# Optimization experiments

Measured on AMD Instinct MI355X. Metric: run time of the kernel, lower is better.

Reference implementation:

```python
import jax, jax.numpy as jnp
import numpy as np

N_NODES = 100000
N_EDGES = 1600000


def setup_inputs() -> dict:
    key = jax.random.key(0)
    ks = jax.random.split(key, 10)
    return {
        "src": jax.random.randint(ks[0], (N_EDGES,), 0, N_NODES, dtype=jnp.int32),
        "dst": jax.random.randint(ks[1], (N_EDGES,), 0, N_NODES, dtype=jnp.int32),
        "logits": jax.random.normal(ks[2], (N_NODES, 64), jnp.float32),
        "features": jax.random.normal(ks[3], (N_NODES, 512), jnp.float32),
        "proj_W": jax.random.normal(ks[4], (512, 128), jnp.float32) * 0.04,
        "proj_b": jnp.zeros((128,), jnp.float32),
        "deg_table": jax.random.normal(ks[5], (512, 64), jnp.float32) * 0.1,
        "W1": jax.random.normal(ks[6], (256, 128), jnp.float32) * 0.06,
        "b1": jnp.zeros((128,), jnp.float32),
        "W2": jax.random.normal(ks[7], (128, 64), jnp.float32) * 0.09,
        "b2": jnp.zeros((64,), jnp.float32),
    }


def _graph_conv(x, W, b, src, dst, out_deg, in_deg, n):
    # DGL GraphConv, norm='both': scale src by out_deg^-1/2, SpMM sum over
    # edges (src -> dst), scale dst by in_deg^-1/2, then bias. Weight is
    # applied before aggregation when in_feats > out_feats (true here).
    cs = jax.lax.rsqrt(jnp.maximum(out_deg, 1.0))  # [N]
    cd = jax.lax.rsqrt(jnp.maximum(in_deg, 1.0))   # [N]
    h = x * cs[:, None]
    if W.shape[0] > W.shape[1]:
        h = h @ W
        agg = jax.ops.segment_sum(h[src], dst, num_segments=n)
    else:
        agg = jax.ops.segment_sum(h[src], dst, num_segments=n) @ W
    return agg * cd[:, None] + b


def reference(src, dst, logits, features, proj_W, proj_b, deg_table, W1, b1, W2, b2):
    n = logits.shape[0]
    ones = jnp.ones(src.shape, jnp.float32)
    out_deg = jax.ops.segment_sum(ones, src, num_segments=n)  # [N]
    in_deg = jax.ops.segment_sum(ones, dst, num_segments=n)   # [N]

    feat = features @ proj_W + proj_b                          # [N, 128]
    deg_idx = (in_deg + out_deg).astype(jnp.int32)             # [N]
    deg_emb = deg_table[deg_idx]                               # [N, 64]
    x = jnp.concatenate([logits, feat, deg_emb], axis=-1)      # [N, 256]

    x = _graph_conv(x, W1, b1, src, dst, out_deg, in_deg, n)
    x = jax.nn.relu(x)  # dropout omitted (eval mode)
    x = _graph_conv(x, W2, b2, src, dst, out_deg, in_deg, n)
    return x
```

## Files before the change

kernel.cpp:

```cpp
#include <hip/hip_runtime.h>
#include <cstdint>
#include <cstddef>


typedef short short8 __attribute__((ext_vector_type(8)));
typedef float f32x4 __attribute__((ext_vector_type(4)));

__device__ __forceinline__ unsigned short f2bf(float f) {
    unsigned u = __float_as_uint(f);
    u += 0x7fff + ((u >> 16) & 1);
    return (unsigned short)(u >> 16);
}
__device__ __forceinline__ float bf2f(unsigned short s) {
    return __uint_as_float(((unsigned)s) << 16);
}

__device__ __forceinline__ void split_f4(float4 a, float4 b, short8& hv, short8& lv) {
    float f[8] = {a.x, a.y, a.z, a.w, b.x, b.y, b.z, b.w};
#pragma unroll
    for (int i = 0; i < 8; ++i) {
        unsigned u = __float_as_uint(f[i]);
        hv[i] = (short)(u >> 16);
        float r = f[i] - __uint_as_float(u & 0xffff0000u);
        lv[i] = (short)(__float_as_uint(r) >> 16);
    }
}


__global__ __launch_bounds__(256) void k_bcount(
    const int* __restrict__ src, const int* __restrict__ dst, int E,
    int* __restrict__ dcount, int* __restrict__ scount)
{
    __shared__ int dh[128], sh_[128];
    int t = threadIdx.x;
    if (t < 128) { dh[t] = 0; sh_[t] = 0; }
    __syncthreads();
    int e0 = blockIdx.x * 4096;
#pragma unroll
    for (int i = 0; i < 16; ++i) {
        int idx = e0 + t + i * 256;
        if (idx < E) {
            atomicAdd(&dh[dst[idx] >> 10], 1);
            atomicAdd(&sh_[src[idx] >> 10], 1);
        }
    }
    __syncthreads();
    if (t < 128) {
        if (dh[t]) atomicAdd(&dcount[t], dh[t]);
        if (sh_[t]) atomicAdd(&scount[t], sh_[t]);
    }
}

__global__ __launch_bounds__(128) void k_bscan(
    const int* __restrict__ dcount, const int* __restrict__ scount, int nb,
    int E, int* __restrict__ dboff, int* __restrict__ sboff,
    int* __restrict__ dcur, int* __restrict__ scur,
    int* __restrict__ rowp, int N)
{
    __shared__ int sh[128];
    int t = threadIdx.x;
    int v = (t < nb) ? dcount[t] : 0;
    sh[t] = v;
    __syncthreads();
    for (int off = 1; off < 128; off <<= 1) {
        int x = (t >= off) ? sh[t - off] : 0;
        __syncthreads();
        sh[t] += x;
        __syncthreads();
    }
    if (t < nb) { int e = sh[t] - v; dboff[t] = e; dcur[t] = e; }
    __syncthreads();
    int v2 = (t < nb) ? scount[t] : 0;
    sh[t] = v2;
    __syncthreads();
    for (int off = 1; off < 128; off <<= 1) {
        int x = (t >= off) ? sh[t - off] : 0;
        __syncthreads();
        sh[t] += x;
        __syncthreads();
    }
    if (t < nb) { int e = sh[t] - v2; sboff[t] = e; scur[t] = e; }
    if (t == 0) rowp[N] = E;
}

__global__ __launch_bounds__(256) void k_scatter2(
    const int* __restrict__ src, const int* __restrict__ dst, int E,
    int* __restrict__ dcur, int* __restrict__ scur,
    unsigned* __restrict__ ebuf, unsigned short* __restrict__ sbuf, int nb)
{
    __shared__ int dh[128], dbase[128], sh_[128], sbase[128];
    int t = threadIdx.x;
    int e0 = blockIdx.x * 4096;
    if (t < 128) { dh[t] = 0; sh_[t] = 0; }
    __syncthreads();
    int s_[16], d_[16];
#pragma unroll
    for (int i = 0; i < 16; ++i) {
        int idx = e0 + t + i * 256;
        if (idx < E) {
            s_[i] = src[idx];
            d_[i] = dst[idx];
            atomicAdd(&dh[d_[i] >> 10], 1);
            atomicAdd(&sh_[s_[i] >> 10], 1);
        } else d_[i] = -1;
    }
    __syncthreads();
    if (t < nb) {
        if (dh[t]) dbase[t] = atomicAdd(&dcur[t], dh[t]);
        if (sh_[t]) sbase[t] = atomicAdd(&scur[t], sh_[t]);
    }
    __syncthreads();
    if (t < 128) { dh[t] = 0; sh_[t] = 0; }
    __syncthreads();
#pragma unroll
    for (int i = 0; i < 16; ++i) {
        if (d_[i] >= 0) {
            int b = d_[i] >> 10;
            int p = dbase[b] + atomicAdd(&dh[b], 1);
            ebuf[p] = (unsigned)s_[i] | ((unsigned)(d_[i] & 1023) << 17);
            int bs = s_[i] >> 10;
            int q = sbase[bs] + atomicAdd(&sh_[bs], 1);
            sbuf[q] = (unsigned short)(s_[i] & 1023);
        }
    }
}

__global__ __launch_bounds__(512) void k_bucket_dst(
    const unsigned* __restrict__ ebuf, const int* __restrict__ dboff,
    const int* __restrict__ dcount, int* __restrict__ ind,
    int* __restrict__ rowp, int* __restrict__ csr, int N)
{
    __shared__ int cnt[1024];
    __shared__ int sums[512];
    int b = blockIdx.x;
    int nb0 = b << 10;
    int ncnt = min(1024, N - nb0);
    int t = threadIdx.x;
    cnt[t] = 0; cnt[t + 512] = 0;
    __syncthreads();
    int lo = dboff[b], hi = lo + dcount[b];
    for (int idx = lo + t; idx < hi; idx += 512)
        atomicAdd(&cnt[ebuf[idx] >> 17], 1);
    __syncthreads();
    int c0 = cnt[2 * t], c1 = cnt[2 * t + 1];
    sums[t] = c0 + c1;
    __syncthreads();
    for (int off = 1; off < 512; off <<= 1) {
        int x = (t >= off) ? sums[t - off] : 0;
        __syncthreads();
        sums[t] += x;
        __syncthreads();
    }
    int excl = sums[t] - (c0 + c1);
    int r0 = lo + excl, r1 = r0 + c0;
    if (2 * t < ncnt)     { rowp[nb0 + 2 * t] = r0;     ind[nb0 + 2 * t] = c0; }
    if (2 * t + 1 < ncnt) { rowp[nb0 + 2 * t + 1] = r1; ind[nb0 + 2 * t + 1] = c1; }
    __syncthreads();
    cnt[2 * t] = r0; cnt[2 * t + 1] = r1;
    __syncthreads();
    for (int idx = lo + t; idx < hi; idx += 512) {
        unsigned e = ebuf[idx];
        int p = atomicAdd(&cnt[e >> 17], 1);
        csr[p] = (int)(e & 0x1FFFF);
    }
}

__global__ __launch_bounds__(512) void k_bucket_src(
    const unsigned short* __restrict__ sbuf, const int* __restrict__ sboff,
    const int* __restrict__ scount, int* __restrict__ outd, int N)
{
    __shared__ int cnt[1024];
    int b = blockIdx.x;
    int nb0 = b << 10;
    int ncnt = min(1024, N - nb0);
    int t = threadIdx.x;
    cnt[t] = 0; cnt[t + 512] = 0;
    __syncthreads();
    int lo = sboff[b], hi = lo + scount[b];
    for (int idx = lo + t; idx < hi; idx += 512)
        atomicAdd(&cnt[sbuf[idx]], 1);
    __syncthreads();
    if (t < ncnt) outd[nb0 + t] = cnt[t];
    if (t + 512 < ncnt) outd[nb0 + t + 512] = cnt[t + 512];
}

__global__ __launch_bounds__(256) void k_norms(
    const int* __restrict__ outd, const int* __restrict__ ind, int N,
    float* __restrict__ cs, float* __restrict__ cd, int* __restrict__ didx)
{
    int i = blockIdx.x * 256 + threadIdx.x;
    if (i < N) {
        int od = outd[i], id = ind[i];
        cs[i] = rsqrtf((float)(od > 0 ? od : 1));
        cd[i] = rsqrtf((float)(id > 0 ? id : 1));
        int d = od + id;
        didx[i] = d > 511 ? 511 : d;
    }
}

__global__ __launch_bounds__(256) void k_wf(
    const float* __restrict__ projW, const float* __restrict__ W1,
    float* __restrict__ WF)
{
    int idx = blockIdx.x * 256 + threadIdx.x;
    int k = idx >> 7, j = idx & 127;
    const float* a = projW + (size_t)k * 128;
    float s = 0.f;
#pragma unroll 8
    for (int m = 0; m < 128; ++m) s = fmaf(a[m], W1[(size_t)(64 + m) * 128 + j], s);
    WF[idx] = s;
}

__global__ void k_cb(const float* __restrict__ projb, const float* __restrict__ W1,
                     float* __restrict__ cb)
{
    int j = threadIdx.x;
    float s = 0.f;
    for (int m = 0; m < 128; ++m) s = fmaf(projb[m], W1[(size_t)(64 + m) * 128 + j], s);
    cb[j] = s;
}

__global__ __launch_bounds__(256) void k_wt1(
    const float* __restrict__ WF, const float* __restrict__ W1,
    unsigned short* __restrict__ wt_hi, unsigned short* __restrict__ wt_lo)
{
    int idx = blockIdx.x * 256 + threadIdx.x;
    int j = idx / 640, k = idx - j * 640;
    float v;
    if (k < 512) v = WF[(size_t)k * 128 + j];
    else if (k < 576) v = W1[(size_t)(k - 512) * 128 + j];
    else v = W1[(size_t)(192 + k - 576) * 128 + j];
    unsigned short h = f2bf(v);
    wt_hi[idx] = h;
    float r = v - bf2f(h);
    wt_lo[idx] = (unsigned short)(__float_as_uint(r) >> 16);
}

__global__ __launch_bounds__(256) void k_wt2(
    const float* __restrict__ W2,
    unsigned short* __restrict__ w2t_hi, unsigned short* __restrict__ w2t_lo)
{
    int idx = blockIdx.x * 256 + threadIdx.x;
    int j = idx >> 7, k = idx & 127;
    float v = W2[(size_t)k * 64 + j];
    unsigned short h = f2bf(v);
    w2t_hi[idx] = h;
    float r = v - bf2f(h);
    w2t_lo[idx] = (unsigned short)(__float_as_uint(r) >> 16);
}

__global__ __launch_bounds__(256, 2) void k_h1(
    const float* __restrict__ logits, const float* __restrict__ features,
    const float* __restrict__ deg_table, const int* __restrict__ didx,
    const unsigned short* __restrict__ wt_hi, const unsigned short* __restrict__ wt_lo,
    const float* __restrict__ cb, const float* __restrict__ cs,
    unsigned short* __restrict__ h1, int N)
{
    constexpr int NT = 20;
    __shared__ __align__(16) short Ah[2][128 * 32];
    __shared__ __align__(16) short Al[2][128 * 32];
    __shared__ __align__(16) short Bh[2][128 * 32];
    __shared__ __align__(16) short Bl[2][128 * 32];
    int tid = threadIdx.x;
    int i0 = blockIdx.x * 128;
    int sr = tid >> 1, shh = tid & 1;
    int snode = i0 + sr; if (snode >= N) snode = N - 1;
    int sdidx = didx[snode];
    int wo0 = sr * 32 + ((shh    ) ^ (sr & 3)) * 8;
    int wo1 = sr * 32 + ((shh + 2) ^ (sr & 3)) * 8;
    int lane = tid & 63, w = tid >> 6;
    int wr = w >> 1, wc = w & 1;
    int fr = lane & 15, kg = lane >> 4;
    int aoff = (wr * 64 + fr) * 32 + (kg ^ (fr & 3)) * 8;
    int boff = (wc * 64 + fr) * 32 + (kg ^ (fr & 3)) * 8;

    f32x4 acc[4][4];
#pragma unroll
    for (int ri = 0; ri < 4; ++ri)
#pragma unroll
        for (int ci = 0; ci < 4; ++ci) acc[ri][ci] = (f32x4)0.f;

    float4 fa0, fa1, fa2, fa3;
    uint4 pbh0, pbh1, pbl0, pbl1;

    auto loadT = [&](int t) {
        const float* ap;
        if (t < 16)      ap = features  + (size_t)snode * 512 + t * 32;
        else if (t < 18) ap = logits    + (size_t)snode * 64 + (t - 16) * 32;
        else             ap = deg_table + (size_t)sdidx * 64 + (t - 18) * 32;
        ap += shh * 8;
        fa0 = *(const float4*)(ap);
        fa1 = *(const float4*)(ap + 4);
        fa2 = *(const float4*)(ap + 16);
        fa3 = *(const float4*)(ap + 20);
        const unsigned short* bh = wt_hi + (size_t)sr * 640 + t * 32 + shh * 8;
        const unsigned short* bl = wt_lo + (size_t)sr * 640 + t * 32 + shh * 8;
        pbh0 = *(const uint4*)(bh);
        pbh1 = *(const uint4*)(bh + 16);
        pbl0 = *(const uint4*)(bl);
        pbl1 = *(const uint4*)(bl + 16);
    };
    auto writeT = [&](int buf) {
        short8 h0, l0, h1v, l1v;
        split_f4(fa0, fa1, h0, l0);
        split_f4(fa2, fa3, h1v, l1v);
        *(short8*)&Ah[buf][wo0] = h0;   *(short8*)&Ah[buf][wo1] = h1v;
        *(short8*)&Al[buf][wo0] = l0;   *(short8*)&Al[buf][wo1] = l1v;
        *(uint4*)&Bh[buf][wo0] = pbh0;  *(uint4*)&Bh[buf][wo1] = pbh1;
        *(uint4*)&Bl[buf][wo0] = pbl0;  *(uint4*)&Bl[buf][wo1] = pbl1;
    };

    loadT(0);
    writeT(0);
    __syncthreads();
    for (int t = 0; t < NT; ++t) {
        if (t + 1 < NT) loadT(t + 1);
        int cbuf = t & 1;
        short8 ah[4], al[4];
#pragma unroll
        for (int ri = 0; ri < 4; ++ri) {
            ah[ri] = *(const short8*)&Ah[cbuf][aoff + ri * 512];
            al[ri] = *(const short8*)&Al[cbuf][aoff + ri * 512];
        }
#pragma unroll
        for (int ci = 0; ci < 4; ++ci) {
            short8 bh = *(const short8*)&Bh[cbuf][boff + ci * 512];
            short8 bl = *(const short8*)&Bl[cbuf][boff + ci * 512];
#pragma unroll
            for (int ri = 0; ri < 4; ++ri) {
                acc[ri][ci] = __builtin_amdgcn_mfma_f32_16x16x32_bf16(ah[ri], bh, acc[ri][ci], 0, 0, 0);
                acc[ri][ci] = __builtin_amdgcn_mfma_f32_16x16x32_bf16(al[ri], bh, acc[ri][ci], 0, 0, 0);
                acc[ri][ci] = __builtin_amdgcn_mfma_f32_16x16x32_bf16(ah[ri], bl, acc[ri][ci], 0, 0, 0);
            }
        }
        if (t + 1 < NT) writeT((t + 1) & 1);
        __syncthreads();
    }

    float cbv[4];
#pragma unroll
    for (int ci = 0; ci < 4; ++ci) cbv[ci] = cb[wc * 64 + ci * 16 + fr];
#pragma unroll
    for (int ri = 0; ri < 4; ++ri) {
#pragma unroll
        for (int j = 0; j < 4; ++j) {
            int row = i0 + wr * 64 + ri * 16 + kg * 4 + j;
            if (row < N) {
                float scv = cs[row];
#pragma unroll
                for (int ci = 0; ci < 4; ++ci) {
                    int col = wc * 64 + ci * 16 + fr;
                    h1[(size_t)row * 128 + col] = f2bf(scv * (acc[ri][ci][j] + cbv[ci]));
                }
            }
        }
    }
}

__global__ __launch_bounds__(256) void k_agg1(
    const unsigned short* __restrict__ h1, const int* __restrict__ rowp,
    const int* __restrict__ csr, const float* __restrict__ cd,
    const float* __restrict__ b1, float* __restrict__ y, int N)
{
    int i = blockIdx.x * 4 + (threadIdx.x >> 6);
    if (i >= N) return;
    int lane = threadIdx.x & 63;
    int s0 = rowp[i], s1 = rowp[i + 1];
    float ax = 0.f, ay = 0.f;
    int e = s0;
    for (; e + 8 <= s1; e += 8) {
        unsigned u0 = *(const unsigned*)(h1 + (size_t)csr[e + 0] * 128 + lane * 2);
        unsigned u1 = *(const unsigned*)(h1 + (size_t)csr[e + 1] * 128 + lane * 2);
        unsigned u2 = *(const unsigned*)(h1 + (size_t)csr[e + 2] * 128 + lane * 2);
        unsigned u3 = *(const unsigned*)(h1 + (size_t)csr[e + 3] * 128 + lane * 2);
        unsigned u4 = *(const unsigned*)(h1 + (size_t)csr[e + 4] * 128 + lane * 2);
        unsigned u5 = *(const unsigned*)(h1 + (size_t)csr[e + 5] * 128 + lane * 2);
        unsigned u6 = *(const unsigned*)(h1 + (size_t)csr[e + 6] * 128 + lane * 2);
        unsigned u7 = *(const unsigned*)(h1 + (size_t)csr[e + 7] * 128 + lane * 2);
        ax += ((__uint_as_float(u0 << 16) + __uint_as_float(u1 << 16)) +
               (__uint_as_float(u2 << 16) + __uint_as_float(u3 << 16))) +
              ((__uint_as_float(u4 << 16) + __uint_as_float(u5 << 16)) +
               (__uint_as_float(u6 << 16) + __uint_as_float(u7 << 16)));
        ay += ((__uint_as_float(u0 & 0xffff0000u) + __uint_as_float(u1 & 0xffff0000u)) +
               (__uint_as_float(u2 & 0xffff0000u) + __uint_as_float(u3 & 0xffff0000u))) +
              ((__uint_as_float(u4 & 0xffff0000u) + __uint_as_float(u5 & 0xffff0000u)) +
               (__uint_as_float(u6 & 0xffff0000u) + __uint_as_float(u7 & 0xffff0000u)));
    }
    for (; e < s1; ++e) {
        unsigned u = *(const unsigned*)(h1 + (size_t)csr[e] * 128 + lane * 2);
        ax += __uint_as_float(u << 16);
        ay += __uint_as_float(u & 0xffff0000u);
    }
    float cdi = cd[i];
    float2 o;
    o.x = fmaxf(fmaf(ax, cdi, b1[lane * 2 + 0]), 0.f);
    o.y = fmaxf(fmaf(ay, cdi, b1[lane * 2 + 1]), 0.f);
    *(float2*)(y + (size_t)i * 128 + lane * 2) = o;
}

__global__ __launch_bounds__(256, 2) void k_h2(
    const float* __restrict__ y,
    const unsigned short* __restrict__ w2t_hi, const unsigned short* __restrict__ w2t_lo,
    const float* __restrict__ cs, unsigned short* __restrict__ h2, int N)
{
    constexpr int NT = 4;
    __shared__ __align__(16) short Ah[2][128 * 32];
    __shared__ __align__(16) short Al[2][128 * 32];
    __shared__ __align__(16) short Bh[2][64 * 32];
    __shared__ __align__(16) short Bl[2][64 * 32];
    int tid = threadIdx.x;
    int i0 = blockIdx.x * 128;
    int sr = tid >> 1, shh = tid & 1;
    int snode = i0 + sr; if (snode >= N) snode = N - 1;
    const float* abase = y + (size_t)snode * 128 + shh * 8;
    int awo0 = sr * 32 + ((shh    ) ^ (sr & 3)) * 8;
    int awo1 = sr * 32 + ((shh + 2) ^ (sr & 3)) * 8;
    int brow_s = tid >> 2, bc = tid & 3;
    int bwo = brow_s * 32 + (bc ^ (brow_s & 3)) * 8;
    int lane = tid & 63, w = tid >> 6;
    int wr = w >> 1, wc = w & 1;
    int fr = lane & 15, kg = lane >> 4;
    int aoff = (wr * 64 + fr) * 32 + (kg ^ (fr & 3)) * 8;
    int boff = (wc * 32 + fr) * 32 + (kg ^ (fr & 3)) * 8;

    f32x4 acc[4][2];
#pragma unroll
    for (int ri = 0; ri < 4; ++ri)
#pragma unroll
        for (int ci = 0; ci < 2; ++ci) acc[ri][ci] = (f32x4)0.f;

    float4 fa0, fa1, fa2, fa3;
    uint4 pbh0, pbl0;

    auto loadT = [&](int t) {
        const float* ap = abase + t * 32;
        fa0 = *(const float4*)(ap);
        fa1 = *(const float4*)(ap + 4);
        fa2 = *(const float4*)(ap + 16);
        fa3 = *(const float4*)(ap + 20);
        pbh0 = *(const uint4*)(w2t_hi + (size_t)brow_s * 128 + t * 32 + bc * 8);
        pbl0 = *(const uint4*)(w2t_lo + (size_t)brow_s * 128 + t * 32 + bc * 8);
    };
    auto writeT = [&](int buf) {
        short8 h0, l0, h1v, l1v;
        split_f4(fa0, fa1, h0, l0);
        split_f4(fa2, fa3, h1v, l1v);
        *(short8*)&Ah[buf][awo0] = h0;  *(short8*)&Ah[buf][awo1] = h1v;
        *(short8*)&Al[buf][awo0] = l0;  *(short8*)&Al[buf][awo1] = l1v;
        *(uint4*)&Bh[buf][bwo] = pbh0;
        *(uint4*)&Bl[buf][bwo] = pbl0;
    };

    loadT(0);
    writeT(0);
    __syncthreads();
    for (int t = 0; t < NT; ++t) {
        if (t + 1 < NT) loadT(t + 1);
        int cbuf = t & 1;
        short8 ah[4], al[4];
#pragma unroll
        for (int ri = 0; ri < 4; ++ri) {
            ah[ri] = *(const short8*)&Ah[cbuf][aoff + ri * 512];
            al[ri] = *(const short8*)&Al[cbuf][aoff + ri * 512];
        }
#pragma unroll
        for (int ci = 0; ci < 2; ++ci) {
            short8 bh = *(const short8*)&Bh[cbuf][boff + ci * 512];
            short8 bl = *(const short8*)&Bl[cbuf][boff + ci * 512];
#pragma unroll
            for (int ri = 0; ri < 4; ++ri) {
                acc[ri][ci] = __builtin_amdgcn_mfma_f32_16x16x32_bf16(ah[ri], bh, acc[ri][ci], 0, 0, 0);
                acc[ri][ci] = __builtin_amdgcn_mfma_f32_16x16x32_bf16(al[ri], bh, acc[ri][ci], 0, 0, 0);
                acc[ri][ci] = __builtin_amdgcn_mfma_f32_16x16x32_bf16(ah[ri], bl, acc[ri][ci], 0, 0, 0);
            }
        }
        if (t + 1 < NT) writeT((t + 1) & 1);
        __syncthreads();
    }

#pragma unroll
    for (int ri = 0; ri < 4; ++ri) {
#pragma unroll
        for (int j = 0; j < 4; ++j) {
            int row = i0 + wr * 64 + ri * 16 + kg * 4 + j;
            if (row < N) {
                float scv = cs[row];
#pragma unroll
                for (int ci = 0; ci < 2; ++ci) {
                    int col = wc * 32 + ci * 16 + fr;
                    h2[(size_t)row * 64 + col] = f2bf(scv * acc[ri][ci][j]);
                }
            }
        }
    }
}

__global__ __launch_bounds__(256) void k_agg2(
    const unsigned short* __restrict__ h2, const int* __restrict__ rowp,
    const int* __restrict__ csr, const float* __restrict__ cd,
    const float* __restrict__ b2, float* __restrict__ out, int N)
{
    int i = blockIdx.x * 8 + (threadIdx.x >> 5);
    if (i >= N) return;
    int lane = threadIdx.x & 31;
    int s0 = rowp[i], s1 = rowp[i + 1];
    float ax = 0.f, ay = 0.f;
    int e = s0;
    for (; e + 8 <= s1; e += 8) {
        unsigned u0 = *(const unsigned*)(h2 + (size_t)csr[e + 0] * 64 + lane * 2);
        unsigned u1 = *(const unsigned*)(h2 + (size_t)csr[e + 1] * 64 + lane * 2);
        unsigned u2 = *(const unsigned*)(h2 + (size_t)csr[e + 2] * 64 + lane * 2);
        unsigned u3 = *(const unsigned*)(h2 + (size_t)csr[e + 3] * 64 + lane * 2);
        unsigned u4 = *(const unsigned*)(h2 + (size_t)csr[e + 4] * 64 + lane * 2);
        unsigned u5 = *(const unsigned*)(h2 + (size_t)csr[e + 5] * 64 + lane * 2);
        unsigned u6 = *(const unsigned*)(h2 + (size_t)csr[e + 6] * 64 + lane * 2);
        unsigned u7 = *(const unsigned*)(h2 + (size_t)csr[e + 7] * 64 + lane * 2);
        ax += ((__uint_as_float(u0 << 16) + __uint_as_float(u1 << 16)) +
               (__uint_as_float(u2 << 16) + __uint_as_float(u3 << 16))) +
              ((__uint_as_float(u4 << 16) + __uint_as_float(u5 << 16)) +
               (__uint_as_float(u6 << 16) + __uint_as_float(u7 << 16)));
        ay += ((__uint_as_float(u0 & 0xffff0000u) + __uint_as_float(u1 & 0xffff0000u)) +
               (__uint_as_float(u2 & 0xffff0000u) + __uint_as_float(u3 & 0xffff0000u))) +
              ((__uint_as_float(u4 & 0xffff0000u) + __uint_as_float(u5 & 0xffff0000u)) +
               (__uint_as_float(u6 & 0xffff0000u) + __uint_as_float(u7 & 0xffff0000u)));
    }
    for (; e < s1; ++e) {
        unsigned u = *(const unsigned*)(h2 + (size_t)csr[e] * 64 + lane * 2);
        ax += __uint_as_float(u << 16);
        ay += __uint_as_float(u & 0xffff0000u);
    }
    float cdi = cd[i];
    float2 o;
    o.x = fmaf(ax, cdi, b2[lane * 2 + 0]);
    o.y = fmaf(ay, cdi, b2[lane * 2 + 1]);
    *(float2*)(out + (size_t)i * 64 + lane * 2) = o;
}

extern "C" void kernel_launch(void* const* d_in, const int* in_sizes, int n_in,
                              void* d_out, int out_size, void* d_ws, size_t ws_size,
                              hipStream_t stream)
{
    const int* src = (const int*)d_in[0];
    const int* dst = (const int*)d_in[1];
    const float* logits = (const float*)d_in[2];
    const float* features = (const float*)d_in[3];
    const float* projW = (const float*)d_in[4];
    const float* projb = (const float*)d_in[5];
    const float* deg_table = (const float*)d_in[6];
    const float* W1 = (const float*)d_in[7];
    const float* b1 = (const float*)d_in[8];
    const float* W2 = (const float*)d_in[9];
    const float* b2 = (const float*)d_in[10];
    const int E = in_sizes[0];
    const int N = in_sizes[2] / 64;

    char* base = (char*)d_ws;
    size_t off = 0;
    auto alloc = [&](size_t bytes) -> void* {
        void* p = base + off;
        off += (bytes + 255) & ~(size_t)255;
        return p;
    };
    int* outd   = (int*)alloc((size_t)N * 4);
    int* ind    = (int*)alloc((size_t)N * 4);
    int* rowp   = (int*)alloc((size_t)(N + 1) * 4);
    int* csr    = (int*)alloc((size_t)E * 4);
    unsigned* ebuf = (unsigned*)alloc((size_t)E * 4);
    unsigned short* sbuf = (unsigned short*)alloc((size_t)E * 2);
    int* didx   = (int*)alloc((size_t)N * 4);
    float* cs   = (float*)alloc((size_t)N * 4);
    float* cd   = (float*)alloc((size_t)N * 4);
    float* WF   = (float*)alloc((size_t)512 * 128 * 4);
    float* cb   = (float*)alloc((size_t)128 * 4);
    int* dcount = (int*)alloc(128 * 4);
    int* scount = (int*)alloc(128 * 4);
    int* dboff  = (int*)alloc(128 * 4);
    int* sboff  = (int*)alloc(128 * 4);
    int* dcur   = (int*)alloc(128 * 4);
    int* scur   = (int*)alloc(128 * 4);
    unsigned short* wt_hi  = (unsigned short*)alloc((size_t)128 * 640 * 2);
    unsigned short* wt_lo  = (unsigned short*)alloc((size_t)128 * 640 * 2);
    unsigned short* w2t_hi = (unsigned short*)alloc((size_t)64 * 128 * 2);
    unsigned short* w2t_lo = (unsigned short*)alloc((size_t)64 * 128 * 2);
    unsigned short* h1 = (unsigned short*)alloc((size_t)N * 128 * 2);
    float* yb   = (float*)alloc((size_t)N * 128 * 4);
    unsigned short* h2 = h1;
    float* outp = (float*)d_out;

    hipMemsetAsync(dcount, 0, 128 * 4, stream);
    hipMemsetAsync(scount, 0, 128 * 4, stream);

    int nb = (N + 255) / 256;
    int mb = (N + 127) / 128;
    int ebk = (E + 4095) / 4096;
    int nbuck = (N + 1023) / 1024;

    k_bcount<<<ebk, 256, 0, stream>>>(src, dst, E, dcount, scount);
    k_bscan<<<1, 128, 0, stream>>>(dcount, scount, nbuck, E, dboff, sboff, dcur, scur, rowp, N);
    k_scatter2<<<ebk, 256, 0, stream>>>(src, dst, E, dcur, scur, ebuf, sbuf, nbuck);
    k_bucket_dst<<<nbuck, 512, 0, stream>>>(ebuf, dboff, dcount, ind, rowp, csr, N);
    k_bucket_src<<<nbuck, 512, 0, stream>>>(sbuf, sboff, scount, outd, N);
    k_norms<<<nb, 256, 0, stream>>>(outd, ind, N, cs, cd, didx);
    k_wf<<<256, 256, 0, stream>>>(projW, W1, WF);
    k_cb<<<1, 128, 0, stream>>>(projb, W1, cb);
    k_wt1<<<320, 256, 0, stream>>>(WF, W1, wt_hi, wt_lo);
    k_wt2<<<32, 256, 0, stream>>>(W2, w2t_hi, w2t_lo);
    k_h1<<<mb, 256, 0, stream>>>(logits, features, deg_table, didx, wt_hi, wt_lo, cb, cs, h1, N);
    k_agg1<<<(N + 3) / 4, 256, 0, stream>>>(h1, rowp, csr, cd, b1, yb, N);
    k_h2<<<mb, 256, 0, stream>>>(yb, w2t_hi, w2t_lo, cs, h2, N);
    k_agg2<<<(N + 7) / 8, 256, 0, stream>>>(h2, rowp, csr, cd, b2, outp, N);
}
```

Before: 345.9 us.

## Drop LDS staging in dense GEMMs; load MFMA fragments directly from global

Both projection GEMM kernels (k_h1, k_h2) are restructured so each wave handles 32 rows across all output columns. The A fragments are loaded straight from global memory into registers in MFMA layout, and B fragments are read directly from the small weight arrays, which should stay cache-resident. This removes the shared-memory double buffering and the block-wide __syncthreads, cutting LDS traffic and barrier stalls. In exchange, A rows are read with a less coalesced pattern, each wave re-reads the weights from cache, and k_h2 loses its occupancy hint in launch bounds.

```diff
diff --git a/kernel.cpp b/kernel.cpp
--- a/kernel.cpp
+++ b/kernel.cpp
@@ -257,100 +257,73 @@
     unsigned short* __restrict__ h1, int N)
 {
     constexpr int NT = 20;
-    __shared__ __align__(16) short Ah[2][128 * 32];
-    __shared__ __align__(16) short Al[2][128 * 32];
-    __shared__ __align__(16) short Bh[2][128 * 32];
-    __shared__ __align__(16) short Bl[2][128 * 32];
     int tid = threadIdx.x;
-    int i0 = blockIdx.x * 128;
-    int sr = tid >> 1, shh = tid & 1;
-    int snode = i0 + sr; if (snode >= N) snode = N - 1;
-    int sdidx = didx[snode];
-    int wo0 = sr * 32 + ((shh    ) ^ (sr & 3)) * 8;
-    int wo1 = sr * 32 + ((shh + 2) ^ (sr & 3)) * 8;
     int lane = tid & 63, w = tid >> 6;
-    int wr = w >> 1, wc = w & 1;
     int fr = lane & 15, kg = lane >> 4;
-    int aoff = (wr * 64 + fr) * 32 + (kg ^ (fr & 3)) * 8;
-    int boff = (wc * 64 + fr) * 32 + (kg ^ (fr & 3)) * 8;
-
-    f32x4 acc[4][4];
-#pragma unroll
-    for (int ri = 0; ri < 4; ++ri)
-#pragma unroll
-        for (int ci = 0; ci < 4; ++ci) acc[ri][ci] = (f32x4)0.f;
-
-    float4 fa0, fa1, fa2, fa3;
-    uint4 pbh0, pbh1, pbl0, pbl1;
-
-    auto loadT = [&](int t) {
-        const float* ap;
-        if (t < 16)      ap = features  + (size_t)snode * 512 + t * 32;
-        else if (t < 18) ap = logits    + (size_t)snode * 64 + (t - 16) * 32;
-        else             ap = deg_table + (size_t)sdidx * 64 + (t - 18) * 32;
-        ap += shh * 8;
-        fa0 = *(const float4*)(ap);
-        fa1 = *(const float4*)(ap + 4);
-        fa2 = *(const float4*)(ap + 16);
-        fa3 = *(const float4*)(ap + 20);
-        const unsigned short* bh = wt_hi + (size_t)sr * 640 + t * 32 + shh * 8;
-        const unsigned short* bl = wt_lo + (size_t)sr * 640 + t * 32 + shh * 8;
-        pbh0 = *(const uint4*)(bh);
-        pbh1 = *(const uint4*)(bh + 16);
-        pbl0 = *(const uint4*)(bl);
-        pbl1 = *(const uint4*)(bl + 16);
+    int i0 = blockIdx.x * 128 + w * 32;
+    int r0 = i0 + fr;       if (r0 >= N) r0 = N - 1;
+    int r1 = i0 + 16 + fr;  if (r1 >= N) r1 = N - 1;
+    int dd0 = didx[r0], dd1 = didx[r1];
+
+    f32x4 acc[2][8];
+#pragma unroll
+    for (int ri = 0; ri < 2; ++ri)
+#pragma unroll
+        for (int ci = 0; ci < 8; ++ci) acc[ri][ci] = (f32x4)0.f;
+
+    auto aptr = [&](int t, int r, int dd) -> const float* {
+        if (t < 16) return features  + (size_t)r * 512 + t * 32 + kg * 8;
+        if (t < 18) return logits    + (size_t)r * 64 + (t - 16) * 32 + kg * 8;
+        return deg_table + (size_t)dd * 64 + (t - 18) * 32 + kg * 8;
     };
-    auto writeT = [&](int buf) {
-        short8 h0, l0, h1v, l1v;
-        split_f4(fa0, fa1, h0, l0);
-        split_f4(fa2, fa3, h1v, l1v);
-        *(short8*)&Ah[buf][wo0] = h0;   *(short8*)&Ah[buf][wo1] = h1v;
-        *(short8*)&Al[buf][wo0] = l0;   *(short8*)&Al[buf][wo1] = l1v;
-        *(uint4*)&Bh[buf][wo0] = pbh0;  *(uint4*)&Bh[buf][wo1] = pbh1;
-        *(uint4*)&Bl[buf][wo0] = pbl0;  *(uint4*)&Bl[buf][wo1] = pbl1;
-    };
-
-    loadT(0);
-    writeT(0);
-    __syncthreads();
+
+    float4 ar00, ar01, ar10, ar11;
+    {
+        const float* p0 = aptr(0, r0, dd0);
+        ar00 = *(const float4*)p0;  ar01 = *(const float4*)(p0 + 4);
+        const float* p1 = aptr(0, r1, dd1);
+        ar10 = *(const float4*)p1;  ar11 = *(const float4*)(p1 + 4);
+    }
+
     for (int t = 0; t < NT; ++t) {
-        if (t + 1 < NT) loadT(t + 1);
-        int cbuf = t & 1;
-        short8 ah[4], al[4];
-#pragma unroll
-        for (int ri = 0; ri < 4; ++ri) {
-            ah[ri] = *(const short8*)&Ah[cbuf][aoff + ri * 512];
-            al[ri] = *(const short8*)&Al[cbuf][aoff + ri * 512];
-        }
-#pragma unroll
-        for (int ci = 0; ci < 4; ++ci) {
-            short8 bh = *(const short8*)&Bh[cbuf][boff + ci * 512];
-            short8 bl = *(const short8*)&Bl[cbuf][boff + ci * 512];
-#pragma unroll
-            for (int ri = 0; ri < 4; ++ri) {
-                acc[ri][ci] = __builtin_amdgcn_mfma_f32_16x16x32_bf16(ah[ri], bh, acc[ri][ci], 0, 0, 0);
-                acc[ri][ci] = __builtin_amdgcn_mfma_f32_16x16x32_bf16(al[ri], bh, acc[ri][ci], 0, 0, 0);
-                acc[ri][ci] = __builtin_amdgcn_mfma_f32_16x16x32_bf16(ah[ri], bl, acc[ri][ci], 0, 0, 0);
-            }
-        }
-        if (t + 1 < NT) writeT((t + 1) & 1);
-        __syncthreads();
-    }
-
-    float cbv[4];
-#pragma unroll
-    for (int ci = 0; ci < 4; ++ci) cbv[ci] = cb[wc * 64 + ci * 16 + fr];
-#pragma unroll
-    for (int ri = 0; ri < 4; ++ri) {
+        short8 ah0, al0, ah1, al1;
+        split_f4(ar00, ar01, ah0, al0);
+        split_f4(ar10, ar11, ah1, al1);
+        if (t + 1 < NT) {
+            const float* p0 = aptr(t + 1, r0, dd0);
+            ar00 = *(const float4*)p0;  ar01 = *(const float4*)(p0 + 4);
+            const float* p1 = aptr(t + 1, r1, dd1);
+            ar10 = *(const float4*)p1;  ar11 = *(const float4*)(p1 + 4);
+        }
+        const unsigned short* bh_base = wt_hi + (size_t)fr * 640 + t * 32 + kg * 8;
+        const unsigned short* bl_base = wt_lo + (size_t)fr * 640 + t * 32 + kg * 8;
+#pragma unroll
+        for (int ci = 0; ci < 8; ++ci) {
+            short8 bh = *(const short8*)(bh_base + (size_t)ci * 16 * 640);
+            short8 bl = *(const short8*)(bl_base + (size_t)ci * 16 * 640);
+            acc[0][ci] = __builtin_amdgcn_mfma_f32_16x16x32_bf16(ah0, bh, acc[0][ci], 0, 0, 0);
+            acc[0][ci] = __builtin_amdgcn_mfma_f32_16x16x32_bf16(al0, bh, acc[0][ci], 0, 0, 0);
+            acc[0][ci] = __builtin_amdgcn_mfma_f32_16x16x32_bf16(ah0, bl, acc[0][ci], 0, 0, 0);
+            acc[1][ci] = __builtin_amdgcn_mfma_f32_16x16x32_bf16(ah1, bh, acc[1][ci], 0, 0, 0);
+            acc[1][ci] = __builtin_amdgcn_mfma_f32_16x16x32_bf16(al1, bh, acc[1][ci], 0, 0, 0);
+            acc[1][ci] = __builtin_amdgcn_mfma_f32_16x16x32_bf16(ah1, bl, acc[1][ci], 0, 0, 0);
+        }
+    }
+
+    float cbv[8];
+#pragma unroll
+    for (int ci = 0; ci < 8; ++ci) cbv[ci] = cb[ci * 16 + fr];
+#pragma unroll
+    for (int ri = 0; ri < 2; ++ri) {
 #pragma unroll
         for (int j = 0; j < 4; ++j) {
-            int row = i0 + wr * 64 + ri * 16 + kg * 4 + j;
+            int row = i0 + ri * 16 + kg * 4 + j;
             if (row < N) {
                 float scv = cs[row];
 #pragma unroll
-                for (int ci = 0; ci < 4; ++ci) {
-                    int col = wc * 64 + ci * 16 + fr;
-                    h1[(size_t)row * 128 + col] = f2bf(scv * (acc[ri][ci][j] + cbv[ci]));
+                for (int ci = 0; ci < 8; ++ci) {
+                    h1[(size_t)row * 128 + ci * 16 + fr] =
+                        f2bf(scv * (acc[ri][ci][j] + cbv[ci]));
                 }
             }
         }
@@ -398,97 +371,67 @@
     *(float2*)(y + (size_t)i * 128 + lane * 2) = o;
 }
 
-__global__ __launch_bounds__(256, 2) void k_h2(
+__global__ __launch_bounds__(256) void k_h2(
     const float* __restrict__ y,
     const unsigned short* __restrict__ w2t_hi, const unsigned short* __restrict__ w2t_lo,
     const float* __restrict__ cs, unsigned short* __restrict__ h2, int N)
 {
     constexpr int NT = 4;
-    __shared__ __align__(16) short Ah[2][128 * 32];
-    __shared__ __align__(16) short Al[2][128 * 32];
-    __shared__ __align__(16) short Bh[2][64 * 32];
-    __shared__ __align__(16) short Bl[2][64 * 32];
     int tid = threadIdx.x;
-    int i0 = blockIdx.x * 128;
-    int sr = tid >> 1, shh = tid & 1;
-    int snode = i0 + sr; if (snode >= N) snode = N - 1;
-    const float* abase = y + (size_t)snode * 128 + shh * 8;
-    int awo0 = sr * 32 + ((shh    ) ^ (sr & 3)) * 8;
-    int awo1 = sr * 32 + ((shh + 2) ^ (sr & 3)) * 8;
-    int brow_s = tid >> 2, bc = tid & 3;
-    int bwo = brow_s * 32 + (bc ^ (brow_s & 3)) * 8;
     int lane = tid & 63, w = tid >> 6;
-    int wr = w >> 1, wc = w & 1;
     int fr = lane & 15, kg = lane >> 4;
-    int aoff = (wr * 64 + fr) * 32 + (kg ^ (fr & 3)) * 8;
-    int boff = (wc * 32 + fr) * 32 + (kg ^ (fr & 3)) * 8;
-
-    f32x4 acc[4][2];
-#pragma unroll
-    for (int ri = 0; ri < 4; ++ri)
-#pragma unroll
-        for (int ci = 0; ci < 2; ++ci) acc[ri][ci] = (f32x4)0.f;
-
-    float4 fa0, fa1, fa2, fa3;
-    uint4 pbh0, pbl0;
-
-    auto loadT = [&](int t) {
-        const float* ap = abase + t * 32;
-        fa0 = *(const float4*)(ap);
-        fa1 = *(const float4*)(ap + 4);
-        fa2 = *(const float4*)(ap + 16);
-        fa3 = *(const float4*)(ap + 20);
-        pbh0 = *(const uint4*)(w2t_hi + (size_t)brow_s * 128 + t * 32 + bc * 8);
-        pbl0 = *(const uint4*)(w2t_lo + (size_t)brow_s * 128 + t * 32 + bc * 8);
-    };
-    auto writeT = [&](int buf) {
-        short8 h0, l0, h1v, l1v;
-        split_f4(fa0, fa1, h0, l0);
-        split_f4(fa2, fa3, h1v, l1v);
-        *(short8*)&Ah[buf][awo0] = h0;  *(short8*)&Ah[buf][awo1] = h1v;
-        *(short8*)&Al[buf][awo0] = l0;  *(short8*)&Al[buf][awo1] = l1v;
-        *(uint4*)&Bh[buf][bwo] = pbh0;
-        *(uint4*)&Bl[buf][bwo] = pbl0;
-    };
-
-    loadT(0);
-    writeT(0);
-    __syncthreads();
+    int i0 = blockIdx.x * 128 + w * 32;
+    int r0 = i0 + fr;       if (r0 >= N) r0 = N - 1;
+    int r1 = i0 + 16 + fr;  if (r1 >= N) r1 = N - 1;
+    const float* a0 = y + (size_t)r0 * 128 + kg * 8;
+    const float* a1 = y + (size_t)r1 * 128 + kg * 8;
+
+    f32x4 acc[2][4];
+#pragma unroll
+    for (int ri = 0; ri < 2; ++ri)
+#pragma unroll
+        for (int ci = 0; ci < 4; ++ci) acc[ri][ci] = (f32x4)0.f;
+
+    float4 ar00 = *(const float4*)(a0);
+    float4 ar01 = *(const float4*)(a0 + 4);
+    float4 ar10 = *(const float4*)(a1);
+    float4 ar11 = *(const float4*)(a1 + 4);
+
     for (int t = 0; t < NT; ++t) {
-        if (t + 1 < NT) loadT(t + 1);
-        int cbuf = t & 1;
-        short8 ah[4], al[4];
-#pragma unroll
-        for (int ri = 0; ri < 4; ++ri) {
-            ah[ri] = *(const short8*)&Ah[cbuf][aoff + ri * 512];
-            al[ri] = *(const short8*)&Al[cbuf][aoff + ri * 512];
-        }
-#pragma unroll
-        for (int ci = 0; ci < 2; ++ci) {
-            short8 bh = *(const short8*)&Bh[cbuf][boff + ci * 512];
-            short8 bl = *(const short8*)&Bl[cbuf][boff + ci * 512];
-#pragma unroll
-            for (int ri = 0; ri < 4; ++ri) {
-                acc[ri][ci] = __builtin_amdgcn_mfma_f32_16x16x32_bf16(ah[ri], bh, acc[ri][ci], 0, 0, 0);
-                acc[ri][ci] = __builtin_amdgcn_mfma_f32_16x16x32_bf16(al[ri], bh, acc[ri][ci], 0, 0, 0);
-                acc[ri][ci] = __builtin_amdgcn_mfma_f32_16x16x32_bf16(ah[ri], bl, acc[ri][ci], 0, 0, 0);
-            }
-        }
-        if (t + 1 < NT) writeT((t + 1) & 1);
-        __syncthreads();
-    }
-
-#pragma unroll
-    for (int ri = 0; ri < 4; ++ri) {
+        short8 ah0, al0, ah1, al1;
+        split_f4(ar00, ar01, ah0, al0);
+        split_f4(ar10, ar11, ah1, al1);
+        if (t + 1 < NT) {
+            ar00 = *(const float4*)(a0 + (t + 1) * 32);
+            ar01 = *(const float4*)(a0 + (t + 1) * 32 + 4);
+            ar10 = *(const float4*)(a1 + (t + 1) * 32);
+            ar11 = *(const float4*)(a1 + (t + 1) * 32 + 4);
+        }
+        const unsigned short* bh_base = w2t_hi + (size_t)fr * 128 + t * 32 + kg * 8;
+        const unsigned short* bl_base = w2t_lo + (size_t)fr * 128 + t * 32 + kg * 8;
+#pragma unroll
+        for (int ci = 0; ci < 4; ++ci) {
+            short8 bh = *(const short8*)(bh_base + (size_t)ci * 16 * 128);
+            short8 bl = *(const short8*)(bl_base + (size_t)ci * 16 * 128);
+            acc[0][ci] = __builtin_amdgcn_mfma_f32_16x16x32_bf16(ah0, bh, acc[0][ci], 0, 0, 0);
+            acc[0][ci] = __builtin_amdgcn_mfma_f32_16x16x32_bf16(al0, bh, acc[0][ci], 0, 0, 0);
+            acc[0][ci] = __builtin_amdgcn_mfma_f32_16x16x32_bf16(ah0, bl, acc[0][ci], 0, 0, 0);
+            acc[1][ci] = __builtin_amdgcn_mfma_f32_16x16x32_bf16(ah1, bh, acc[1][ci], 0, 0, 0);
+            acc[1][ci] = __builtin_amdgcn_mfma_f32_16x16x32_bf16(al1, bh, acc[1][ci], 0, 0, 0);
+            acc[1][ci] = __builtin_amdgcn_mfma_f32_16x16x32_bf16(ah1, bl, acc[1][ci], 0, 0, 0);
+        }
+    }
+
+#pragma unroll
+    for (int ri = 0; ri < 2; ++ri) {
 #pragma unroll
         for (int j = 0; j < 4; ++j) {
-            int row = i0 + wr * 64 + ri * 16 + kg * 4 + j;
+            int row = i0 + ri * 16 + kg * 4 + j;
             if (row < N) {
                 float scv = cs[row];
 #pragma unroll
-                for (int ci = 0; ci < 2; ++ci) {
-                    int col = wc * 32 + ci * 16 + fr;
-                    h2[(size_t)row * 64 + col] = f2bf(scv * acc[ri][ci][j]);
+                for (int ci = 0; ci < 4; ++ci) {
+                    h2[(size_t)row * 64 + ci * 16 + fr] = f2bf(scv * acc[ri][ci][j]);
                 }
             }
         }
```

After: 469.9 us. 1.36x slower.
